# Kernel optimization log

Measured on AMD Instinct MI355X. Metric: run time of the kernel, lower is better.

The kernel has to match this reference:

```python
import jax, jax.numpy as jnp
import numpy as np

N = 50000   # nodes
E = 800000  # edges
F_IN = 512
H = 128     # per-hop hidden width
ORDER = 3   # hops (iterations 1..3)
C = 16      # classes


def spmm(idx, vals, x):
    """Sparse [N,N] @ dense [N,d] via COO edges: out[r] += vals[e] * x[c]."""
    row, col = idx[0], idx[1]
    return jax.ops.segment_sum(vals[:, None] * x[col], row, num_segments=x.shape[0])


def setup_inputs() -> dict:
    key = jax.random.key(0)
    ks = jax.random.split(key, 9)
    x = jax.random.normal(ks[0], (N, F_IN), jnp.float32)
    adj_indices = jax.random.randint(ks[1], (2, E), 0, N)
    adj_values = jax.random.uniform(ks[2], (E,), jnp.float32)
    w1 = jax.random.normal(ks[3], (ORDER, F_IN, H), jnp.float32) * 0.05
    b1 = jax.random.normal(ks[4], (ORDER, 1, H), jnp.float32) * 0.05
    w2 = jax.random.normal(ks[5], (ORDER, ORDER * H, H), jnp.float32) * 0.05
    b2 = jax.random.normal(ks[6], (ORDER, 1, H), jnp.float32) * 0.05
    wf = jax.random.normal(ks[7], (ORDER * H, C), jnp.float32) * 0.05
    bf = jnp.zeros((C,), jnp.float32)
    return dict(x=x, adj_indices=adj_indices, adj_values=adj_values,
                w1=w1, b1=b1, w2=w2, b2=b2, wf=wf, bf=bf)


def reference(x, adj_indices, adj_values, w1, b1, w2, b2, wf, bf):
    # Upper: SparseNGCNLayer_i (iterations = i+1): XW + b -> relu -> (i) spmm hops.
    # Dropout is identity in eval mode.
    feats1 = []
    for i in range(ORDER):
        h = jax.nn.relu(x @ w1[i] + b1[i])  # [N, H]
        for _ in range(i):
            h = spmm(adj_indices, adj_values, h)
        feats1.append(h)
    a1 = jnp.concatenate(feats1, axis=1)  # [N, 3H]

    # Bottom: DenseNGCNLayer_i: AW -> (i) spmm hops -> + bias.
    feats2 = []
    for i in range(ORDER):
        h = a1 @ w2[i]  # [N, H]
        for _ in range(i):
            h = spmm(adj_indices, adj_values, h)
        feats2.append(h + b2[i])
    a2 = jnp.concatenate(feats2, axis=1)  # [N, 3H]

    return jax.nn.log_softmax(a2 @ wf + bf, axis=1)  # [N, C]
```

## Files before the change

### kernel.cpp

```cpp
#include <hip/hip_runtime.h>
#include <hip/hip_bf16.h>
#include <cstdint>
#include <cstddef>

#define N_NODES 50000
#define N_EDGES 800000
#define FIN 512
#define HW_ 128
#define NCLS 16
#define SCAN_NB 196

typedef __attribute__((ext_vector_type(4))) float floatx4;
typedef __attribute__((ext_vector_type(4))) int int4v;
typedef __bf16 bf16x8 __attribute__((ext_vector_type(8)));

__device__ __forceinline__ void glds16(const __bf16* g, __bf16* l) {
  __builtin_amdgcn_global_load_lds(
      (const __attribute__((address_space(1))) void*)g,
      (__attribute__((address_space(3))) void*)l, 16, 0, 0);
}

__global__ __launch_bounds__(256) void k_rank(const int* __restrict__ idx,
                                              int* __restrict__ cnt,
                                              int* __restrict__ rank) {
  int e = blockIdx.x * 1024 + threadIdx.x;
#pragma unroll
  for (int u = 0; u < 4; u++) {
    int ee = e + u * 256;
    if (ee < N_EDGES) rank[ee] = atomicAdd(&cnt[idx[ee]], 1);
  }
}

#define PREP_NT1 48
#define PREP_NU 120
__global__ __launch_bounds__(256) void k_prep(
    const float* __restrict__ w1, __bf16* __restrict__ w1t,
    const float* __restrict__ w2, const float* __restrict__ wf,
    __bf16* __restrict__ Ut,
    const float* __restrict__ b2, const float* __restrict__ bfv,
    float* __restrict__ cc) {
  int b = blockIdx.x;
  int tid = threadIdx.x;
  if (b < PREP_NT1) {
    int tb = b;
    const int K = FIN;
    int tilesK = K >> 6;
    int i = tb / (tilesK * 2);
    int rr = tb - i * tilesK * 2;
    int kt = rr >> 1;
    int nt = rr & 1;
    const float* wS = w1 + (size_t)i * K * 128;
    __bf16* wtS = w1t + (size_t)i * 128 * K;
    int k0 = kt * 64, n0 = nt * 64;
    __shared__ float tile[64][65];
    int tc = tid & 63, tr = tid >> 6;
#pragma unroll
    for (int q = 0; q < 16; q++) {
      int row = tr + q * 4;
      tile[row][tc] = wS[(size_t)(k0 + row) * 128 + n0 + tc];
    }
    __syncthreads();
#pragma unroll
    for (int q = 0; q < 16; q++) {
      int nr = tr + q * 4;
      wtS[(size_t)(n0 + nr) * K + k0 + tc] = (__bf16)tile[tc][nr];
    }
  } else if (b < PREP_NT1 + PREP_NU) {
    int t = (b - PREP_NT1) * 256 + tid;
    int col = t / 384;
    int q = t - col * 384;
    int p = col >> 4, c = col & 15;
    int j = q >> 7;
    int i = p - j;
    float val = 0.f;
    if (i >= 0 && i <= 2) {
      const float* w2row = w2 + ((size_t)i * 384 + q) * 128;
      const float* wfcol = wf + (size_t)128 * i * NCLS + c;
      for (int m = 0; m < 128; m++) val += w2row[m] * wfcol[m * NCLS];
    }
    Ut[(size_t)col * 384 + q] = (__bf16)val;
  } else {
    int c = tid;
    if (c < NCLS) {
      float s = bfv[c];
      for (int k = 0; k < 384; k++) s += b2[k] * wf[k * NCLS + c];
      cc[c] = s;
    }
  }
}

__global__ __launch_bounds__(256) void k_scan_block(const int* __restrict__ cnt,
                                                    int* __restrict__ bsum) {
  int t = blockIdx.x * 256 + threadIdx.x;
  int v = (t < N_NODES) ? cnt[t] : 0;
#pragma unroll
  for (int o = 32; o >= 1; o >>= 1) v += __shfl_down(v, o);
  __shared__ int ws[4];
  if ((threadIdx.x & 63) == 0) ws[threadIdx.x >> 6] = v;
  __syncthreads();
  if (threadIdx.x == 0) bsum[blockIdx.x] = ws[0] + ws[1] + ws[2] + ws[3];
}

__global__ __launch_bounds__(256) void k_scan_fill(const int* __restrict__ cnt,
                                                   const int* __restrict__ bsum,
                                                   int* __restrict__ rowptr) {
  int tid = threadIdx.x;
  int lane = tid & 63;
  int pv = (tid < blockIdx.x && tid < SCAN_NB) ? bsum[tid] : 0;
#pragma unroll
  for (int o = 32; o >= 1; o >>= 1) pv += __shfl_down(pv, o);
  __shared__ int ps[4];
  if (lane == 0) ps[tid >> 6] = pv;
  int t = blockIdx.x * 256 + tid;
  int c = (t < N_NODES) ? cnt[t] : 0;
  int v = c;
#pragma unroll
  for (int o = 1; o < 64; o <<= 1) {
    int n = __shfl_up(v, o);
    if (lane >= o) v += n;
  }
  __shared__ int wt[4];
  if (lane == 63) wt[tid >> 6] = v;
  __syncthreads();
  int add = ps[0] + ps[1] + ps[2] + ps[3];
  for (int w = 0; w < (tid >> 6); w++) add += wt[w];
  int ex = v - c + add;
  if (t < N_NODES) rowptr[t] = ex;
  if (t == 0) rowptr[N_NODES] = N_EDGES;
}

__global__ __launch_bounds__(256) void k_place(
    const int* __restrict__ idx, const float* __restrict__ vals,
    const int* __restrict__ rank, const int* __restrict__ rowptr,
    int2* __restrict__ epack) {
  int e = blockIdx.x * 256 + threadIdx.x;
  if (e < N_EDGES) {
    int r = idx[e];
    int c = idx[N_EDGES + e];
    int p = rowptr[r] + rank[e];
    epack[p] = make_int2(c, __float_as_int(vals[e]));
  }
}

__global__ __launch_bounds__(256) void gemm1(
    const float* __restrict__ A,
    const __bf16* __restrict__ Bt,
    const float* __restrict__ bias,
    __bf16* __restrict__ hb) {
  const int M = N_NODES, K = FIN;
  __shared__ __align__(16) __bf16 sA[128 * 32];
  __shared__ __align__(16) __bf16 sB[128 * 32];
  int tid = threadIdx.x;
  int m0 = blockIdx.x * 128;
  int blk = blockIdx.y;
  const __bf16* Bblk = Bt + (size_t)blk * 128 * K;
  int wave = tid >> 6, lane = tid & 63;
  int wm = (wave & 1) * 64, wn = (wave >> 1) * 64;
  floatx4 acc[4][4] = {};

  int rA = lane >> 2;
  int gch = (lane & 3) ^ ((lane >> 3) & 3);
  int r0 = wave * 32 + rA;
  int r1 = r0 + 16;
  int gm0 = m0 + r0; gm0 = (gm0 < M) ? gm0 : (M - 1);
  int gm1 = m0 + r1; gm1 = (gm1 < M) ? gm1 : (M - 1);
  const float* pa0 = A + (size_t)gm0 * K + gch * 8;
  const float* pa1 = A + (size_t)gm1 * K + gch * 8;
  const __bf16* pb0 = Bblk + (size_t)r0 * K + gch * 8;
  const __bf16* pb1 = Bblk + (size_t)r1 * K + gch * 8;
  __bf16* lA0 = sA + wave * 1024 + lane * 8;
  __bf16* lA1 = sA + wave * 1024 + 512 + lane * 8;
  __bf16* lB0 = sB + wave * 1024;
  __bf16* lB1 = sB + wave * 1024 + 512;

  int fm = lane & 15, fg = lane >> 4;
  int sloto = (fg ^ ((fm >> 1) & 3)) * 8;

  for (int k0 = 0; k0 < K; k0 += 32) {
    floatx4 x0a = *(const floatx4*)(pa0 + k0);
    floatx4 x0b = *(const floatx4*)(pa0 + k0 + 4);
    floatx4 x1a = *(const floatx4*)(pa1 + k0);
    floatx4 x1b = *(const floatx4*)(pa1 + k0 + 4);
    __syncthreads();
    glds16(pb0 + k0, lB0);
    glds16(pb1 + k0, lB1);
    union { bf16x8 v; int4v i; } u0, u1;
#pragma unroll
    for (int q = 0; q < 4; q++) {
      u0.v[q] = (__bf16)x0a[q]; u0.v[q + 4] = (__bf16)x0b[q];
      u1.v[q] = (__bf16)x1a[q]; u1.v[q + 4] = (__bf16)x1b[q];
    }
    *(int4v*)lA0 = u0.i;
    *(int4v*)lA1 = u1.i;
    __syncthreads();

    bf16x8 af[4], bfr[4];
#pragma unroll
    for (int mt = 0; mt < 4; mt++)
      af[mt] = *(const bf16x8*)(sA + (wm + mt * 16 + fm) * 32 + sloto);
#pragma unroll
    for (int nt = 0; nt < 4; nt++)
      bfr[nt] = *(const bf16x8*)(sB + (wn + nt * 16 + fm) * 32 + sloto);
#pragma unroll
    for (int mt = 0; mt < 4; mt++)
#pragma unroll
      for (int nt = 0; nt < 4; nt++)
        acc[mt][nt] = __builtin_amdgcn_mfma_f32_16x16x32_bf16(af[mt], bfr[nt], acc[mt][nt], 0, 0, 0);
  }

  int colb = lane & 15, rbase = (lane >> 4) << 2;
#pragma unroll
  for (int mt = 0; mt < 4; mt++)
#pragma unroll
    for (int r = 0; r < 4; r++) {
      int gm = m0 + wm + mt * 16 + rbase + r;
      if (gm >= M) continue;
#pragma unroll
      for (int nt = 0; nt < 4; nt++) {
        int gc = blk * 128 + wn + nt * 16 + colb;
        float vv = acc[mt][nt][r] + bias[gc];
        vv = fmaxf(vv, 0.f);
        hb[(size_t)gm * 384 + gc] = (__bf16)vv;
      }
    }
}

__global__ __launch_bounds__(256) void k_sgemm(
    const __bf16* __restrict__ hb,
    const __bf16* __restrict__ Ut,
    float* __restrict__ S,
    float* __restrict__ R4) {
  const int M = N_NODES;
  int wave = threadIdx.x >> 6, lane = threadIdx.x & 63;
  int fm = lane & 15, fg = lane >> 4;
  int m0 = blockIdx.x * 128 + wave * 32;
  floatx4 acc[2][5] = {};
  int r0 = m0 + fm;      r0 = (r0 < M) ? r0 : (M - 1);
  int r1 = m0 + 16 + fm; r1 = (r1 < M) ? r1 : (M - 1);
  const __bf16* pa0 = hb + (size_t)r0 * 384 + fg * 8;
  const __bf16* pa1 = hb + (size_t)r1 * 384 + fg * 8;
  const __bf16* pb = Ut + (size_t)fm * 384 + fg * 8;
#pragma unroll 2
  for (int k0 = 0; k0 < 384; k0 += 32) {
    bf16x8 a0 = *(const bf16x8*)(pa0 + k0);
    bf16x8 a1 = *(const bf16x8*)(pa1 + k0);
#pragma unroll
    for (int nt = 0; nt < 5; nt++) {
      bf16x8 bv = *(const bf16x8*)(pb + (size_t)nt * 16 * 384 + k0);
      acc[0][nt] = __builtin_amdgcn_mfma_f32_16x16x32_bf16(a0, bv, acc[0][nt], 0, 0, 0);
      acc[1][nt] = __builtin_amdgcn_mfma_f32_16x16x32_bf16(a1, bv, acc[1][nt], 0, 0, 0);
    }
  }
  int colb = lane & 15, rbase = (lane >> 4) << 2;
#pragma unroll
  for (int mt = 0; mt < 2; mt++)
#pragma unroll
    for (int r = 0; r < 4; r++) {
      int gm = m0 + mt * 16 + rbase + r;
      if (gm >= M) continue;
#pragma unroll
      for (int nt = 0; nt < 4; nt++)
        S[(size_t)gm * 64 + nt * 16 + colb] = acc[mt][nt][r];
      R4[(size_t)gm * 16 + colb] = acc[mt][4][r];
    }
}

template <bool FINAL>
__global__ __launch_bounds__(256) void k_hop(
    const int* __restrict__ rowptr, const int2* __restrict__ epack,
    const float* __restrict__ Rin,
    const float* __restrict__ S, int sofs,
    float* __restrict__ Rout,
    const float* __restrict__ cc) {
  int tid = threadIdx.x;
  int grp = tid >> 4, l = tid & 15;
  int row = blockIdx.x * 16 + grp;
  if (row >= N_NODES) return;
  int s = rowptr[row], e = rowptr[row + 1];
  float a = S[(size_t)row * 64 + sofs + l];
  for (int i = s; i < e; i += 16) {
    int take = e - i; if (take > 16) take = 16;
    int2 ed = (l < take) ? epack[i + l] : make_int2(0, 0);
    int j = 0;
    for (; j + 4 <= take; j += 4) {
      int c0 = __shfl(ed.x, j, 16), c1 = __shfl(ed.x, j + 1, 16);
      int c2 = __shfl(ed.x, j + 2, 16), c3 = __shfl(ed.x, j + 3, 16);
      float v0 = __int_as_float(__shfl(ed.y, j, 16));
      float v1 = __int_as_float(__shfl(ed.y, j + 1, 16));
      float v2 = __int_as_float(__shfl(ed.y, j + 2, 16));
      float v3 = __int_as_float(__shfl(ed.y, j + 3, 16));
      float g0 = Rin[(size_t)c0 * 16 + l];
      float g1 = Rin[(size_t)c1 * 16 + l];
      float g2 = Rin[(size_t)c2 * 16 + l];
      float g3 = Rin[(size_t)c3 * 16 + l];
      a += v0 * g0 + v1 * g1 + v2 * g2 + v3 * g3;
    }
    for (; j < take; j++) {
      int c0 = __shfl(ed.x, j, 16);
      float v0 = __int_as_float(__shfl(ed.y, j, 16));
      a += v0 * Rin[(size_t)c0 * 16 + l];
    }
  }
  if (!FINAL) {
    Rout[(size_t)row * 16 + l] = a;
  } else {
    a += cc[l];
    float m = a;
#pragma unroll
    for (int o = 8; o >= 1; o >>= 1) m = fmaxf(m, __shfl_xor(m, o, 16));
    float sm = expf(a - m);
#pragma unroll
    for (int o = 8; o >= 1; o >>= 1) sm += __shfl_xor(sm, o, 16);
    Rout[(size_t)row * 16 + l] = (a - m) - logf(sm);
  }
}

extern "C" void kernel_launch(void* const* d_in, const int* in_sizes, int n_in,
                              void* d_out, int out_size, void* d_ws, size_t ws_size,
                              hipStream_t stream) {
  const float* x   = (const float*)d_in[0];
  const int*   adj = (const int*)d_in[1];
  const float* av  = (const float*)d_in[2];
  const float* w1  = (const float*)d_in[3];
  const float* b1  = (const float*)d_in[4];
  const float* w2  = (const float*)d_in[5];
  const float* b2  = (const float*)d_in[6];
  const float* wf  = (const float*)d_in[7];
  const float* bf  = (const float*)d_in[8];
  float* out = (float*)d_out;

  char* ws = (char*)d_ws;
  size_t off = 0;
  auto alloc = [&](size_t bytes) -> void* {
    off = (off + 255) & ~(size_t)255;
    void* p = ws + off;
    off += bytes;
    return p;
  };

  float* S    = (float*)alloc((size_t)N_NODES * 64 * 4);
  float* R4   = (float*)alloc((size_t)N_NODES * 16 * 4);
  float* RA   = (float*)alloc((size_t)N_NODES * 16 * 4);
  float* RB   = (float*)alloc((size_t)N_NODES * 16 * 4);
  __bf16* hb  = (__bf16*)alloc((size_t)N_NODES * 384 * 2);
  __bf16* w1t = (__bf16*)alloc((size_t)3 * 128 * FIN * 2);
  __bf16* Ut  = (__bf16*)alloc((size_t)80 * 384 * 2);
  int* rowptr = (int*)alloc((size_t)(N_NODES + 1) * 4);
  int* cnt    = (int*)alloc((size_t)N_NODES * 4);
  int* bsum   = (int*)alloc((size_t)SCAN_NB * 4);
  int* rankv  = (int*)alloc((size_t)N_EDGES * 4);
  int2* epack = (int2*)alloc((size_t)N_EDGES * 8);
  float* cc   = (float*)alloc(64);

  hipMemsetAsync(cnt, 0, (size_t)N_NODES * 4, stream);
  k_rank<<<(N_EDGES + 1023) / 1024, 256, 0, stream>>>(adj, cnt, rankv);
  k_prep<<<PREP_NT1 + PREP_NU + 1, 256, 0, stream>>>(
      w1, w1t, w2, wf, Ut, b2, bf, cc);
  k_scan_block<<<SCAN_NB, 256, 0, stream>>>(cnt, bsum);
  k_scan_fill<<<SCAN_NB, 256, 0, stream>>>(cnt, bsum, rowptr);
  k_place<<<(N_EDGES + 255) / 256, 256, 0, stream>>>(adj, av, rankv, rowptr, epack);

  dim3 g1((N_NODES + 127) / 128, 3);
  gemm1<<<g1, 256, 0, stream>>>(x, w1t, b1, hb);

  k_sgemm<<<(N_NODES + 127) / 128, 256, 0, stream>>>(hb, Ut, S, R4);

  int hop_grid = (N_NODES + 15) / 16;
  k_hop<false><<<hop_grid, 256, 0, stream>>>(rowptr, epack, R4, S, 48, RB, cc);
  k_hop<false><<<hop_grid, 256, 0, stream>>>(rowptr, epack, RB, S, 32, RA, cc);
  k_hop<false><<<hop_grid, 256, 0, stream>>>(rowptr, epack, RA, S, 16, RB, cc);
  k_hop<true><<<hop_grid, 256, 0, stream>>>(rowptr, epack, RB, S, 0, out, cc);
}
```

Measured before the change: 351.9 us.

## Double-buffer gemm1 LDS tiles and remap blocks so XCDs share A rows

```diff
diff --git a/kernel.cpp b/kernel.cpp
--- a/kernel.cpp
+++ b/kernel.cpp
@@ -142,17 +142,23 @@
   }
 }
 
+#define G1_TRIOS 391
+#define G1_TPX 49
 __global__ __launch_bounds__(256) void gemm1(
     const float* __restrict__ A,
     const __bf16* __restrict__ Bt,
     const float* __restrict__ bias,
     __bf16* __restrict__ hb) {
   const int M = N_NODES, K = FIN;
-  __shared__ __align__(16) __bf16 sA[128 * 32];
-  __shared__ __align__(16) __bf16 sB[128 * 32];
+  __shared__ __align__(16) __bf16 sA[2 * 128 * 32];
+  __shared__ __align__(16) __bf16 sB[2 * 128 * 32];
   int tid = threadIdx.x;
-  int m0 = blockIdx.x * 128;
-  int blk = blockIdx.y;
+  int id = blockIdx.x;
+  int xcd = id & 7, slot = id >> 3;
+  int trio = xcd * G1_TPX + slot / 3;
+  int blk = slot - (slot / 3) * 3;
+  if (trio >= G1_TRIOS) return;
+  int m0 = trio * 128;
   const __bf16* Bblk = Bt + (size_t)blk * 128 * K;
   int wave = tid >> 6, lane = tid & 63;
   int wm = (wave & 1) * 64, wn = (wave >> 1) * 64;
@@ -168,39 +174,73 @@
   const float* pa1 = A + (size_t)gm1 * K + gch * 8;
   const __bf16* pb0 = Bblk + (size_t)r0 * K + gch * 8;
   const __bf16* pb1 = Bblk + (size_t)r1 * K + gch * 8;
-  __bf16* lA0 = sA + wave * 1024 + lane * 8;
-  __bf16* lA1 = sA + wave * 1024 + 512 + lane * 8;
-  __bf16* lB0 = sB + wave * 1024;
-  __bf16* lB1 = sB + wave * 1024 + 512;
+  int lofsA = wave * 1024 + lane * 8;
+  int lofsB = wave * 1024;
 
   int fm = lane & 15, fg = lane >> 4;
   int sloto = (fg ^ ((fm >> 1) & 3)) * 8;
 
-  for (int k0 = 0; k0 < K; k0 += 32) {
-    floatx4 x0a = *(const floatx4*)(pa0 + k0);
-    floatx4 x0b = *(const floatx4*)(pa0 + k0 + 4);
-    floatx4 x1a = *(const floatx4*)(pa1 + k0);
-    floatx4 x1b = *(const floatx4*)(pa1 + k0 + 4);
-    __syncthreads();
-    glds16(pb0 + k0, lB0);
-    glds16(pb1 + k0, lB1);
+  {
+    floatx4 x0a = *(const floatx4*)(pa0);
+    floatx4 x0b = *(const floatx4*)(pa0 + 4);
+    floatx4 x1a = *(const floatx4*)(pa1);
+    floatx4 x1b = *(const floatx4*)(pa1 + 4);
+    glds16(pb0, sB + lofsB);
+    glds16(pb1, sB + lofsB + 512);
     union { bf16x8 v; int4v i; } u0, u1;
 #pragma unroll
     for (int q = 0; q < 4; q++) {
       u0.v[q] = (__bf16)x0a[q]; u0.v[q + 4] = (__bf16)x0b[q];
       u1.v[q] = (__bf16)x1a[q]; u1.v[q + 4] = (__bf16)x1b[q];
     }
-    *(int4v*)lA0 = u0.i;
-    *(int4v*)lA1 = u1.i;
+    *(int4v*)(sA + lofsA) = u0.i;
+    *(int4v*)(sA + lofsA + 512) = u1.i;
+  }
+  __syncthreads();
+
+  for (int t = 0; t < 15; t++) {
+    int cb = (t & 1) * 4096;
+    int nb = cb ^ 4096;
+    int k1 = t * 32 + 32;
+    floatx4 n0a = *(const floatx4*)(pa0 + k1);
+    floatx4 n0b = *(const floatx4*)(pa0 + k1 + 4);
+    floatx4 n1a = *(const floatx4*)(pa1 + k1);
+    floatx4 n1b = *(const floatx4*)(pa1 + k1 + 4);
+    glds16(pb0 + k1, sB + nb + lofsB);
+    glds16(pb1 + k1, sB + nb + lofsB + 512);
+
+    bf16x8 af[4], bfr[4];
+#pragma unroll
+    for (int mt = 0; mt < 4; mt++)
+      af[mt] = *(const bf16x8*)(sA + cb + (wm + mt * 16 + fm) * 32 + sloto);
+#pragma unroll
+    for (int nt = 0; nt < 4; nt++)
+      bfr[nt] = *(const bf16x8*)(sB + cb + (wn + nt * 16 + fm) * 32 + sloto);
+#pragma unroll
+    for (int mt = 0; mt < 4; mt++)
+#pragma unroll
+      for (int nt = 0; nt < 4; nt++)
+        acc[mt][nt] = __builtin_amdgcn_mfma_f32_16x16x32_bf16(af[mt], bfr[nt], acc[mt][nt], 0, 0, 0);
+
+    union { bf16x8 v; int4v i; } u0, u1;
+#pragma unroll
+    for (int q = 0; q < 4; q++) {
+      u0.v[q] = (__bf16)n0a[q]; u0.v[q + 4] = (__bf16)n0b[q];
+      u1.v[q] = (__bf16)n1a[q]; u1.v[q + 4] = (__bf16)n1b[q];
+    }
+    *(int4v*)(sA + nb + lofsA) = u0.i;
+    *(int4v*)(sA + nb + lofsA + 512) = u1.i;
     __syncthreads();
-
+  }
+  {
+    int cb = 4096;
     bf16x8 af[4], bfr[4];
 #pragma unroll
     for (int mt = 0; mt < 4; mt++)
-      af[mt] = *(const bf16x8*)(sA + (wm + mt * 16 + fm) * 32 + sloto);
+      af[mt] = *(const bf16x8*)(sA + cb + (wm + mt * 16 + fm) * 32 + sloto);
 #pragma unroll
     for (int nt = 0; nt < 4; nt++)
-      bfr[nt] = *(const bf16x8*)(sB + (wn + nt * 16 + fm) * 32 + sloto);
+      bfr[nt] = *(const bf16x8*)(sB + cb + (wn + nt * 16 + fm) * 32 + sloto);
 #pragma unroll
     for (int mt = 0; mt < 4; mt++)
 #pragma unroll
@@ -360,8 +400,7 @@
   k_scan_fill<<<SCAN_NB, 256, 0, stream>>>(cnt, bsum, rowptr);
   k_place<<<(N_EDGES + 255) / 256, 256, 0, stream>>>(adj, av, rankv, rowptr, epack);
 
-  dim3 g1((N_NODES + 127) / 128, 3);
-  gemm1<<<g1, 256, 0, stream>>>(x, w1t, b1, hb);
+  gemm1<<<8 * G1_TPX * 3, 256, 0, stream>>>(x, w1t, b1, hb);
 
   k_sgemm<<<(N_NODES + 127) / 128, 256, 0, stream>>>(hb, Ut, S, R4);
 
```

After: 349.3 us. No clear change (-0.7%).

## Load gemm1 MFMA fragments directly from global and group row-tile trios per XCD

Applied to the files above, without the earlier changes.

```diff
diff --git a/kernel.cpp b/kernel.cpp
--- a/kernel.cpp
+++ b/kernel.cpp
@@ -13,12 +13,6 @@
 typedef __attribute__((ext_vector_type(4))) float floatx4;
 typedef __attribute__((ext_vector_type(4))) int int4v;
 typedef __bf16 bf16x8 __attribute__((ext_vector_type(8)));
-
-__device__ __forceinline__ void glds16(const __bf16* g, __bf16* l) {
-  __builtin_amdgcn_global_load_lds(
-      (const __attribute__((address_space(1))) void*)g,
-      (__attribute__((address_space(3))) void*)l, 16, 0, 0);
-}
 
 __global__ __launch_bounds__(256) void k_rank(const int* __restrict__ idx,
                                               int* __restrict__ cnt,
@@ -142,70 +136,73 @@
   }
 }
 
+#define G1_TRIOS 391
+#define G1_TPX 49
 __global__ __launch_bounds__(256) void gemm1(
     const float* __restrict__ A,
     const __bf16* __restrict__ Bt,
     const float* __restrict__ bias,
     __bf16* __restrict__ hb) {
   const int M = N_NODES, K = FIN;
-  __shared__ __align__(16) __bf16 sA[128 * 32];
-  __shared__ __align__(16) __bf16 sB[128 * 32];
   int tid = threadIdx.x;
-  int m0 = blockIdx.x * 128;
-  int blk = blockIdx.y;
+  int id = blockIdx.x;
+  int xcd = id & 7, slot = id >> 3;
+  int trio = xcd * G1_TPX + slot / 3;
+  int blk = slot - (slot / 3) * 3;
+  if (trio >= G1_TRIOS) return;
+  int m0 = trio * 128;
   const __bf16* Bblk = Bt + (size_t)blk * 128 * K;
   int wave = tid >> 6, lane = tid & 63;
   int wm = (wave & 1) * 64, wn = (wave >> 1) * 64;
+  int fm = lane & 15, fg = lane >> 4;
   floatx4 acc[4][4] = {};
 
-  int rA = lane >> 2;
-  int gch = (lane & 3) ^ ((lane >> 3) & 3);
-  int r0 = wave * 32 + rA;
-  int r1 = r0 + 16;
-  int gm0 = m0 + r0; gm0 = (gm0 < M) ? gm0 : (M - 1);
-  int gm1 = m0 + r1; gm1 = (gm1 < M) ? gm1 : (M - 1);
-  const float* pa0 = A + (size_t)gm0 * K + gch * 8;
-  const float* pa1 = A + (size_t)gm1 * K + gch * 8;
-  const __bf16* pb0 = Bblk + (size_t)r0 * K + gch * 8;
-  const __bf16* pb1 = Bblk + (size_t)r1 * K + gch * 8;
-  __bf16* lA0 = sA + wave * 1024 + lane * 8;
-  __bf16* lA1 = sA + wave * 1024 + 512 + lane * 8;
-  __bf16* lB0 = sB + wave * 1024;
-  __bf16* lB1 = sB + wave * 1024 + 512;
-
-  int fm = lane & 15, fg = lane >> 4;
-  int sloto = (fg ^ ((fm >> 1) & 3)) * 8;
-
+  const float* pa0;
+  const float* pa1;
+  const float* pa2;
+  const float* pa3;
+  {
+    int g0 = m0 + wm + 0 * 16 + fm; g0 = (g0 < M) ? g0 : (M - 1);
+    int g1 = m0 + wm + 1 * 16 + fm; g1 = (g1 < M) ? g1 : (M - 1);
+    int g2 = m0 + wm + 2 * 16 + fm; g2 = (g2 < M) ? g2 : (M - 1);
+    int g3 = m0 + wm + 3 * 16 + fm; g3 = (g3 < M) ? g3 : (M - 1);
+    pa0 = A + (size_t)g0 * K + fg * 8;
+    pa1 = A + (size_t)g1 * K + fg * 8;
+    pa2 = A + (size_t)g2 * K + fg * 8;
+    pa3 = A + (size_t)g3 * K + fg * 8;
+  }
+  const __bf16* pb0 = Bblk + (size_t)(wn + 0 * 16 + fm) * K + fg * 8;
+  const __bf16* pb1 = Bblk + (size_t)(wn + 1 * 16 + fm) * K + fg * 8;
+  const __bf16* pb2 = Bblk + (size_t)(wn + 2 * 16 + fm) * K + fg * 8;
+  const __bf16* pb3 = Bblk + (size_t)(wn + 3 * 16 + fm) * K + fg * 8;
+
+#pragma unroll 2
   for (int k0 = 0; k0 < K; k0 += 32) {
-    floatx4 x0a = *(const floatx4*)(pa0 + k0);
-    floatx4 x0b = *(const floatx4*)(pa0 + k0 + 4);
-    floatx4 x1a = *(const floatx4*)(pa1 + k0);
-    floatx4 x1b = *(const floatx4*)(pa1 + k0 + 4);
-    __syncthreads();
-    glds16(pb0 + k0, lB0);
-    glds16(pb1 + k0, lB1);
-    union { bf16x8 v; int4v i; } u0, u1;
+    bf16x8 afr[4], bfr[4];
+    floatx4 lo0 = *(const floatx4*)(pa0 + k0);
+    floatx4 hi0 = *(const floatx4*)(pa0 + k0 + 4);
+    floatx4 lo1 = *(const floatx4*)(pa1 + k0);
+    floatx4 hi1 = *(const floatx4*)(pa1 + k0 + 4);
+    floatx4 lo2 = *(const floatx4*)(pa2 + k0);
+    floatx4 hi2 = *(const floatx4*)(pa2 + k0 + 4);
+    floatx4 lo3 = *(const floatx4*)(pa3 + k0);
+    floatx4 hi3 = *(const floatx4*)(pa3 + k0 + 4);
+    bfr[0] = *(const bf16x8*)(pb0 + k0);
+    bfr[1] = *(const bf16x8*)(pb1 + k0);
+    bfr[2] = *(const bf16x8*)(pb2 + k0);
+    bfr[3] = *(const bf16x8*)(pb3 + k0);
 #pragma unroll
     for (int q = 0; q < 4; q++) {
-      u0.v[q] = (__bf16)x0a[q]; u0.v[q + 4] = (__bf16)x0b[q];
-      u1.v[q] = (__bf16)x1a[q]; u1.v[q + 4] = (__bf16)x1b[q];
-    }
-    *(int4v*)lA0 = u0.i;
-    *(int4v*)lA1 = u1.i;
-    __syncthreads();
-
-    bf16x8 af[4], bfr[4];
+      afr[0][q] = (__bf16)lo0[q]; afr[0][q + 4] = (__bf16)hi0[q];
+      afr[1][q] = (__bf16)lo1[q]; afr[1][q + 4] = (__bf16)hi1[q];
+      afr[2][q] = (__bf16)lo2[q]; afr[2][q + 4] = (__bf16)hi2[q];
+      afr[3][q] = (__bf16)lo3[q]; afr[3][q + 4] = (__bf16)hi3[q];
+    }
 #pragma unroll
     for (int mt = 0; mt < 4; mt++)
-      af[mt] = *(const bf16x8*)(sA + (wm + mt * 16 + fm) * 32 + sloto);
-#pragma unroll
-    for (int nt = 0; nt < 4; nt++)
-      bfr[nt] = *(const bf16x8*)(sB + (wn + nt * 16 + fm) * 32 + sloto);
-#pragma unroll
-    for (int mt = 0; mt < 4; mt++)
 #pragma unroll
       for (int nt = 0; nt < 4; nt++)
-        acc[mt][nt] = __builtin_amdgcn_mfma_f32_16x16x32_bf16(af[mt], bfr[nt], acc[mt][nt], 0, 0, 0);
+        acc[mt][nt] = __builtin_amdgcn_mfma_f32_16x16x32_bf16(afr[mt], bfr[nt], acc[mt][nt], 0, 0, 0);
   }
 
   int colb = lane & 15, rbase = (lane >> 4) << 2;
@@ -360,8 +357,7 @@
   k_scan_fill<<<SCAN_NB, 256, 0, stream>>>(cnt, bsum, rowptr);
   k_place<<<(N_EDGES + 255) / 256, 256, 0, stream>>>(adj, av, rankv, rowptr, epack);
 
-  dim3 g1((N_NODES + 127) / 128, 3);
-  gemm1<<<g1, 256, 0, stream>>>(x, w1t, b1, hb);
+  gemm1<<<8 * G1_TPX * 3, 256, 0, stream>>>(x, w1t, b1, hb);
 
   k_sgemm<<<(N_NODES + 127) / 128, 256, 0, stream>>>(hb, Ut, S, R4);
 
```

Measured after the change: 444.8 us. +26.4%, slower.
